# Kernel optimization log

Hardware: AMD Instinct MI355X
Metric: run time of the kernel (lower is better)

The kernel has to match this reference:

```python
import jax, jax.numpy as jnp
import numpy as np
import math

B, S, D, H, DFF = 2, 2048, 1024, 16, 4096
DK = D // H
EPS = 1e-5

def layer_norm(x, g, b):
    mu = jnp.mean(x, axis=-1, keepdims=True)
    var = jnp.mean(jnp.square(x - mu), axis=-1, keepdims=True)
    return (x - mu) * jax.lax.rsqrt(var + EPS) * g + b

def setup_inputs() -> dict:
    key = jax.random.key(0)
    ks = jax.random.split(key, 12)
    p = lambda k, shape: (jax.random.normal(k, shape, jnp.float32) * 0.02)
    return {
        "x": jax.random.normal(ks[0], (B, S, D), jnp.float32),
        "mask": jax.random.randint(ks[1], (B, S, S), 0, 2).astype(bool),
        "Wq": p(ks[2], (D, D)), "bq": jnp.zeros((D,), jnp.float32),
        "Wk": p(ks[3], (D, D)), "bk": jnp.zeros((D,), jnp.float32),
        "Wv": p(ks[4], (D, D)), "bv": jnp.zeros((D,), jnp.float32),
        "Wo": p(ks[5], (D, D)), "bo": jnp.zeros((D,), jnp.float32),
        "W1": p(ks[6], (DFF, D)), "b1": jnp.zeros((DFF,), jnp.float32),
        "W2": p(ks[7], (D, DFF)), "b2": jnp.zeros((D,), jnp.float32),
        "g_attn": jnp.ones((D,), jnp.float32), "b_attn": jnp.zeros((D,), jnp.float32),
        "g_ffn": jnp.ones((D,), jnp.float32), "b_ffn": jnp.zeros((D,), jnp.float32),
    }

def reference(x, mask, Wq, bq, Wk, bk, Wv, bv, Wo, bo, W1, b1, W2, b2, g_attn, b_attn, g_ffn, b_ffn):
    orig_dtype = x.dtype
    nx = layer_norm(x, g_attn, b_attn)
    # project and split heads: [B,S,D] -> [B,H,S,DK]
    split = lambda t: t.reshape(B, S, H, DK).transpose(0, 2, 1, 3)
    q = split(nx @ Wq.T + bq)
    k = split(nx @ Wk.T + bk)
    v = split(nx @ Wv.T + bv)
    # explicit fp32 upcast as in the original
    scores = jnp.einsum('bhqd,bhkd->bhqk', q.astype(jnp.float32), k.astype(jnp.float32)) / math.sqrt(DK)
    scores = jnp.where(mask[:, None, :, :], jnp.float32(-10000.0), scores)
    attn = jax.nn.softmax(scores, axis=-1)
    context = jnp.einsum('bhqk,bhkd->bhqd', attn, v.astype(jnp.float32)).astype(orig_dtype)
    context = context.transpose(0, 2, 1, 3).reshape(B, S, D)
    x = x + (context @ Wo.T + bo)
    nx = layer_norm(x, g_ffn, b_ffn)
    h = jax.nn.gelu(nx @ W1.T + b1, approximate=False)  # torch F.gelu default is exact erf
    x = x + (h @ W2.T + b2)
    return x
```

## Files before the change

### kernel.cpp

```cpp
#include <hip/hip_runtime.h>
#include <stdint.h>

#define B_ 2
#define S_ 2048
#define D_ 1024
#define H_ 16
#define DK_ 64
#define DFF_ 4096
#define M_ (B_*S_)

typedef __bf16 bf16x8 __attribute__((ext_vector_type(8)));
typedef float  f32x4  __attribute__((ext_vector_type(4)));

__device__ __forceinline__ unsigned short f2bf(float f) {
    union { float f; unsigned int u; } x; x.f = f;
    unsigned int r = x.u + 0x7FFFu + ((x.u >> 16) & 1u);
    return (unsigned short)(r >> 16);
}
__device__ __forceinline__ float bf2f(unsigned short h) {
    union { unsigned int u; float f; } x; x.u = ((unsigned int)h) << 16;
    return x.f;
}

__device__ __forceinline__ void gl16(const void* g, void* l) {
    __builtin_amdgcn_global_load_lds((const __attribute__((address_space(1))) unsigned int*)g,
                                     (__attribute__((address_space(3))) unsigned int*)l, 16, 0, 0);
}

static constexpr size_t OFS_XC   = 256;
static constexpr size_t OFS_MASK = OFS_XC   + 8388608;
static constexpr size_t OFS_WQKV = OFS_MASK + 8388608;
static constexpr size_t OFS_WO   = OFS_WQKV + 6291456;
static constexpr size_t OFS_W1   = OFS_WO   + 2097152;
static constexpr size_t OFS_W2   = OFS_W1   + 8388608;
static constexpr size_t OFS_BIAS = OFS_W2   + 8388608;
static constexpr size_t OFS_S0   = OFS_BIAS + 53248;
static constexpr size_t OFS_S1   = OFS_S0   + 8388608;
static constexpr size_t OFS_S2   = OFS_S1   + 8388608;
static constexpr size_t OFS_S3   = OFS_S2   + 8388608;
static constexpr size_t OFS_H    = OFS_S3   + 8388608;

#define BOF_QKV 0
#define BOF_O   3072
#define BOF_2   4096
#define BOF_GA  5120
#define BOF_BA  6144
#define BOF_GF  7168
#define BOF_BF  8192
#define BOF_1   9216

struct Parts { float* p[4]; };

__global__ void detect_kernel(const unsigned int* __restrict__ g_attn,
                              const unsigned int* __restrict__ mask,
                              int* __restrict__ flags) {
    const int u = threadIdx.x;
    unsigned int w0 = mask[u], w1 = mask[64 + u];
    bool a32  = (w0 <= 1u) && (w1 <= 1u);
    bool af32 = ((w0 == 0u) || (w0 == 0x3F800000u)) && ((w1 == 0u) || (w1 == 0x3F800000u));
    bool a8 = true;
    #pragma unroll
    for (int j = 0; j < 4; j++)
        a8 = a8 && (((w0 >> (8*j)) & 0xFFu) <= 1u) && (((w1 >> (8*j)) & 0xFFu) <= 1u);
    int all32 = __all(a32), all8 = __all(a8), allf32 = __all(af32);
    if (u == 0) {
        unsigned int g0 = g_attn[0];
        int fm = (g0 == 0x3F800000u) ? 0 : ((g0 == 0x3C003C00u) ? 2 : 1);
        int mm = all32 ? 0 : (all8 ? 1 : (allf32 ? 2 : 3));
        flags[0] = fm; flags[1] = mm;
    }
}

struct BigSrc { const void* s[7]; };

__device__ __forceinline__ void conv4(const void* src, size_t si,
                                      unsigned short* dst, size_t di, int fm) {
    ushort4 ov;
    if (fm == 1) {
        ov = *(const ushort4*)((const unsigned short*)src + si);
    } else if (fm == 0) {
        const float* fp = (const float*)src + si;
        float4 f = *(const float4*)fp;
        ov.x = f2bf(f.x); ov.y = f2bf(f.y); ov.z = f2bf(f.z); ov.w = f2bf(f.w);
    } else {
        const _Float16* hp = (const _Float16*)src + si;
        ov.x = f2bf((float)hp[0]); ov.y = f2bf((float)hp[1]);
        ov.z = f2bf((float)hp[2]); ov.w = f2bf((float)hp[3]);
    }
    *(ushort4*)(dst + di) = ov;
}

__global__ __launch_bounds__(256) void convert_big_kernel(BigSrc srcs, char* ws) {
    const int fm = ((const int*)ws)[0];
    size_t i = ((size_t)blockIdx.x * 256 + threadIdx.x) * 4;
    if (i >= 16777216) return;
    if (i < 4194304) {
        conv4(srcs.s[0], i, (unsigned short*)(ws + OFS_XC), i, fm);
    } else if (i < 7340032) {
        size_t off = i - 4194304;
        int sub = (int)(off >> 20);
        size_t loc = off & 1048575;
        conv4(srcs.s[1 + sub], loc, (unsigned short*)(ws + OFS_WQKV), off, fm);
    } else if (i < 8388608) {
        size_t off = i - 7340032;
        conv4(srcs.s[4], off, (unsigned short*)(ws + OFS_WO), off, fm);
    } else if (i < 12582912) {
        size_t off = i - 8388608;
        conv4(srcs.s[5], off, (unsigned short*)(ws + OFS_W1), off, fm);
    } else {
        size_t off = i - 12582912;
        conv4(srcs.s[6], off, (unsigned short*)(ws + OFS_W2), off, fm);
    }
}

struct SmallSrc { const void* s[10]; };

__global__ __launch_bounds__(256) void convert_small_kernel(SmallSrc srcs, char* ws) {
    int idx = blockIdx.x * 256 + threadIdx.x;
    if (idx >= 13312) return;
    const int fm = ((const int*)ws)[0];
    int seg = idx >> 10; if (seg > 9) seg = 9;
    int loc = idx - seg * 1024;
    const void* s = srcs.s[seg];
    float f;
    if (fm == 1)      f = bf2f(((const unsigned short*)s)[loc]);
    else if (fm == 0) f = ((const float*)s)[loc];
    else              f = (float)((const _Float16*)s)[loc];
    ((float*)(ws + OFS_BIAS))[idx] = f;
}

__global__ __launch_bounds__(256) void mask_bits_kernel(const void* msrc, char* ws) {
    const int mm = ((const int*)ws)[1];
    size_t e = (size_t)blockIdx.x * 256 + threadIdx.x;
    bool p;
    if (mm == 0)      p = ((const int*)msrc)[e] != 0;
    else if (mm == 1) p = ((const unsigned char*)msrc)[e] != 0;
    else if (mm == 2) p = ((const unsigned int*)msrc)[e] != 0;
    else              p = ((const unsigned short*)msrc)[e] != 0;
    unsigned long long bal = __ballot(p);
    if ((threadIdx.x & 63) == 0)
        ((unsigned long long*)(ws + OFS_MASK))[e >> 6] = bal;
}

template<int IN32>
__global__ __launch_bounds__(256) void ln_kernel(const void* __restrict__ xin,
                                                 const float* __restrict__ g,
                                                 const float* __restrict__ b,
                                                 unsigned short* __restrict__ out) {
    const int row = blockIdx.x;
    const int t = threadIdx.x;
    float f0, f1, f2, f3;
    if (IN32) {
        const float* xr = (const float*)xin + (size_t)row * D_;
        float4 xv = *(const float4*)(xr + t * 4);
        f0 = xv.x; f1 = xv.y; f2 = xv.z; f3 = xv.w;
    } else {
        const unsigned short* xr = (const unsigned short*)xin + (size_t)row * D_;
        ushort4 xv = *(const ushort4*)(xr + t * 4);
        f0 = bf2f(xv.x); f1 = bf2f(xv.y); f2 = bf2f(xv.z); f3 = bf2f(xv.w);
    }
    float s = f0 + f1 + f2 + f3;
    float q = f0*f0 + f1*f1 + f2*f2 + f3*f3;
    for (int m = 1; m < 64; m <<= 1) { s += __shfl_xor(s, m); q += __shfl_xor(q, m); }
    __shared__ float red[8];
    __shared__ float mv[2];
    int w = t >> 6, u = t & 63;
    if (u == 0) { red[w*2] = s; red[w*2+1] = q; }
    __syncthreads();
    if (t == 0) {
        float S = red[0] + red[2] + red[4] + red[6];
        float Q = red[1] + red[3] + red[5] + red[7];
        float mu = S * (1.0f / D_);
        float var = Q * (1.0f / D_) - mu * mu;
        mv[0] = mu; mv[1] = rsqrtf(var + 1e-5f);
    }
    __syncthreads();
    float mu = mv[0], r = mv[1];
    int i = t * 4;
    ushort4 ov;
    ov.x = f2bf((f0 - mu) * r * g[i]   + b[i]);
    ov.y = f2bf((f1 - mu) * r * g[i+1] + b[i+1]);
    ov.z = f2bf((f2 - mu) * r * g[i+2] + b[i+2]);
    ov.w = f2bf((f3 - mu) * r * g[i+3] + b[i+3]);
    *(ushort4*)(out + (size_t)row * D_ + i) = ov;
}

template<int EPI>
__global__ __launch_bounds__(256) void gemm_bt_kernel(
    const unsigned short* __restrict__ A,
    const unsigned short* __restrict__ Bm,
    const float* __restrict__ bias,
    void* __restrict__ out,
    float* __restrict__ p1,
    unsigned short* __restrict__ q_out,
    unsigned short* __restrict__ k_out,
    unsigned short* __restrict__ vT_out,
    int M, int N, int K, int Kstride)
{
    __shared__ __attribute__((aligned(16))) unsigned short ldsA[2][4096];
    __shared__ __attribute__((aligned(16))) unsigned short ldsB[2][4096];
    const int t = threadIdx.x;
    const int w = t >> 6, u = t & 63, quad = u >> 4, l15 = u & 15;
    const int bx = blockIdx.x, by = blockIdx.y;
    const int z = (EPI == 5) ? blockIdx.z : 0;

    const int c0 = t, c1 = t + 256;
    const int ar0 = by*128 + ((c0 >> 6) << 4) + (c0 & 15), ak0 = ((c0 >> 4) & 3) * 8;
    const int ar1 = by*128 + ((c1 >> 6) << 4) + (c1 & 15), ak1 = ((c1 >> 4) & 3) * 8;
    const int br0 = bx*128 + ((c0 >> 6) << 4) + (c0 & 15);
    const int br1 = bx*128 + ((c1 >> 6) << 4) + (c1 & 15);
    const size_t kofs = (size_t)z * K;
    const unsigned short* pa0 = A  + (size_t)ar0 * Kstride + kofs + ak0;
    const unsigned short* pa1 = A  + (size_t)ar1 * Kstride + kofs + ak1;
    const unsigned short* pb0 = Bm + (size_t)br0 * Kstride + kofs + ak0;
    const unsigned short* pb1 = Bm + (size_t)br1 * Kstride + kofs + ak1;

    const int cbase0 = (w * 64) * 8;
    const int cbase1 = (256 + w * 64) * 8;

    f32x4 acc[4][4];
    #pragma unroll
    for (int i = 0; i < 4; i++)
        #pragma unroll
        for (int j = 0; j < 4; j++) acc[i][j] = (f32x4){0.f, 0.f, 0.f, 0.f};

    const int mbase = (w >> 1) * 4;
    const int nbase = (w & 1) * 4;

    for (int k0 = 0; k0 < K; k0 += 64) {
        __syncthreads();
        gl16(pa0,      &ldsA[0][cbase0]);
        gl16(pa1,      &ldsA[0][cbase1]);
        gl16(pb0,      &ldsB[0][cbase0]);
        gl16(pb1,      &ldsB[0][cbase1]);
        gl16(pa0 + 32, &ldsA[1][cbase0]);
        gl16(pa1 + 32, &ldsA[1][cbase1]);
        gl16(pb0 + 32, &ldsB[1][cbase0]);
        gl16(pb1 + 32, &ldsB[1][cbase1]);
        pa0 += 64; pa1 += 64; pb0 += 64; pb1 += 64;
        __syncthreads();
        #pragma unroll
        for (int sub = 0; sub < 2; sub++) {
            bf16x8 af[4], bfr[4];
            #pragma unroll
            for (int mt = 0; mt < 4; mt++) af[mt]  = *(const bf16x8*)&ldsA[sub][((mbase+mt)*64 + u) * 8];
            #pragma unroll
            for (int nt = 0; nt < 4; nt++) bfr[nt] = *(const bf16x8*)&ldsB[sub][((nbase+nt)*64 + u) * 8];
            #pragma unroll
            for (int mt = 0; mt < 4; mt++)
                #pragma unroll
                for (int nt = 0; nt < 4; nt++)
                    acc[mt][nt] = __builtin_amdgcn_mfma_f32_16x16x32_bf16(af[mt], bfr[nt], acc[mt][nt], 0, 0, 0);
        }
    }

    #pragma unroll
    for (int mt = 0; mt < 4; mt++) {
        #pragma unroll
        for (int nt = 0; nt < 4; nt++) {
            const int m0 = by*128 + (w >> 1)*64 + mt*16 + quad*4;
            const int n  = bx*128 + (w & 1)*64 + nt*16 + l15;
            float bn = 0.f;
            if constexpr (EPI != 5) bn = bias[n];
            float val[4];
            #pragma unroll
            for (int r = 0; r < 4; r++) val[r] = acc[mt][nt][r] + bn;
            if constexpr (EPI == 1) {
                #pragma unroll
                for (int r = 0; r < 4; r++) {
                    float v = val[r];
                    float ge = 0.5f * v * (1.0f + erff(v * 0.70710678118654752f));
                    ((unsigned short*)out)[(size_t)(m0 + r) * N + n] = f2bf(ge);
                }
            } else if constexpr (EPI == 2) {
                int sel = n >> 10, nn = n & 1023;
                int hh = nn >> 6, dk = nn & 63;
                int bb = m0 >> 11, ss = m0 & 2047;
                if (sel < 2) {
                    unsigned short* dst = sel == 0 ? q_out : k_out;
                    #pragma unroll
                    for (int r = 0; r < 4; r++)
                        dst[(((size_t)bb * H_ + hh) * S_ + ss + r) * DK_ + dk] = f2bf(val[r]);
                } else {
                    ushort4 pk;
                    pk.x = f2bf(val[0]); pk.y = f2bf(val[1]);
                    pk.z = f2bf(val[2]); pk.w = f2bf(val[3]);
                    *(ushort4*)&vT_out[(((size_t)bb * H_ + hh) * DK_ + dk) * S_ + ss] = pk;
                }
            } else {
                float* dst = z ? p1 : (float*)out;
                #pragma unroll
                for (int r = 0; r < 4; r++)
                    dst[(size_t)(m0 + r) * N + n] = val[r];
            }
        }
    }
}

template<int EPI>
__global__ __launch_bounds__(512, 2) void gemm256_kernel(
    const unsigned short* __restrict__ A,
    const unsigned short* __restrict__ Bm,
    const float* __restrict__ bias,
    void* __restrict__ out,
    unsigned short* __restrict__ q_out,
    unsigned short* __restrict__ k_out,
    unsigned short* __restrict__ vT_out,
    Parts parts,
    int N, int K, int Kstride)
{
    __shared__ __attribute__((aligned(16))) unsigned short sh[2][2][16384];
    const int t = threadIdx.x, w = t >> 6, u = t & 63, quad = u >> 4, l15 = u & 15;
    const int wm = w >> 2, wn = w & 3;
    const int bx = blockIdx.x, by = blockIdx.y;
    const int z = (EPI == 5) ? blockIdx.z : 0;
    const size_t kofs = (size_t)z * K;

    const int r1 = t >> 3, cc1 = t & 7, cs1 = cc1 ^ (r1 & 7);
    const unsigned short* srcA = A  + ((size_t)by * 256 + r1) * Kstride + kofs + cs1 * 8;
    const unsigned short* srcB = Bm + ((size_t)bx * 256 + r1) * Kstride + kofs + cs1 * 8;
    const size_t halfstep = 128 * (size_t)Kstride;
    const size_t rowstep64 = 64 * (size_t)Kstride;

    const int rowA = wm * 16 + l15;
    const int rowB = wn * 16 + l15;
    const int cx0 = ((quad    ) ^ (l15 & 7)) * 8;
    const int cx1 = ((quad + 4) ^ (l15 & 7)) * 8;

    f32x4 acc[8][4];
    #pragma unroll
    for (int i = 0; i < 8; i++)
        #pragma unroll
        for (int j = 0; j < 4; j++) acc[i][j] = (f32x4){0.f, 0.f, 0.f, 0.f};

#define STAGE(bufi, mat, half, tile) { \
    const unsigned short* _s = ((mat) ? srcB : srcA) + (size_t)(half) * halfstep + (size_t)(tile) * 64; \
    unsigned short* _d = &sh[bufi][mat][(half) * 8192 + w * 512]; \
    gl16(_s, _d); gl16(_s + rowstep64, _d + 4096); }

#define LOAD_A(bufi, mh) { \
    const unsigned short* _p = &sh[bufi][0][0]; \
    _Pragma("unroll") \
    for (int f = 0; f < 4; f++) { \
        aF[f][0] = *(const bf16x8*)&_p[((mh) * 128 + f * 32 + rowA) * 64 + cx0]; \
        aF[f][1] = *(const bf16x8*)&_p[((mh) * 128 + f * 32 + rowA) * 64 + cx1]; \
    } }

#define LOAD_B(bufi, nh) { \
    const unsigned short* _p = &sh[bufi][1][0]; \
    _Pragma("unroll") \
    for (int g = 0; g < 2; g++) { \
        bF[nh][g][0] = *(const bf16x8*)&_p[((nh) * 128 + g * 64 + rowB) * 64 + cx0]; \
        bF[nh][g][1] = *(const bf16x8*)&_p[((nh) * 128 + g * 64 + rowB) * 64 + cx1]; \
    } }

#define QUADC(mh, nh) \
    __builtin_amdgcn_s_setprio(1); \
    _Pragma("unroll") \
    for (int ks = 0; ks < 2; ks++) \
        _Pragma("unroll") \
        for (int f = 0; f < 4; f++) \
            _Pragma("unroll") \
            for (int g = 0; g < 2; g++) \
                acc[(mh)*4 + f][(nh)*2 + g] = __builtin_amdgcn_mfma_f32_16x16x32_bf16( \
                    aF[f][ks], bF[nh][g][ks], acc[(mh)*4 + f][(nh)*2 + g], 0, 0, 0); \
    __builtin_amdgcn_s_setprio(0);

#define BARR __builtin_amdgcn_s_barrier()
#define VM6  asm volatile("s_waitcnt vmcnt(6)" ::: "memory")

    STAGE(0, 0, 0, 0);
    STAGE(0, 1, 0, 0);
    STAGE(0, 0, 1, 0);
    STAGE(0, 1, 1, 0);
    STAGE(1, 0, 0, 1);
    STAGE(1, 1, 0, 1);
    STAGE(1, 0, 1, 1);
    VM6;
    BARR;

    bf16x8 aF[4][2];
    bf16x8 bF[2][2][2];

    const int nIt = K >> 7;
    const int lastT = (K >> 6) - 1;

    #pragma unroll 1
    for (int it = 0; it < nIt; ++it) {
        const int t1 = 2 * it + 1;
        const int t2 = (it < nIt - 1) ? 2 * it + 2 : lastT;
        const int t3 = (it < nIt - 1) ? 2 * it + 3 : lastT;

        LOAD_A(0, 0); LOAD_B(0, 0);
        STAGE(1, 1, 1, t1);
        BARR; QUADC(0, 0); BARR;
        LOAD_B(0, 1);
        STAGE(0, 0, 0, t2);
        BARR; QUADC(0, 1); BARR;
        LOAD_A(0, 1);
        STAGE(0, 1, 0, t2);
        BARR; QUADC(1, 0); BARR;
        STAGE(0, 0, 1, t2);
        VM6;
        BARR; QUADC(1, 1); BARR;
        LOAD_A(1, 0); LOAD_B(1, 0);
        STAGE(0, 1, 1, t2);
        BARR; QUADC(0, 0); BARR;
        LOAD_B(1, 1);
        STAGE(1, 0, 0, t3);
        BARR; QUADC(0, 1); BARR;
        LOAD_A(1, 1);
        STAGE(1, 1, 0, t3);
        BARR; QUADC(1, 0); BARR;
        STAGE(1, 0, 1, t3);
        VM6;
        BARR; QUADC(1, 1); BARR;
    }
    asm volatile("s_waitcnt vmcnt(0)" ::: "memory");

#undef STAGE
#undef LOAD_A
#undef LOAD_B
#undef QUADC
#undef BARR
#undef VM6

    if constexpr (EPI == 1) {
        #pragma unroll
        for (int f = 0; f < 8; f++) {
            #pragma unroll
            for (int g = 0; g < 4; g++) {
                const int m0 = by * 256 + f * 32 + wm * 16 + quad * 4;
                const int n  = bx * 256 + g * 64 + wn * 16 + l15;
                const float bn = bias[n];
                #pragma unroll
                for (int r = 0; r < 4; r++) {
                    float v = acc[f][g][r] + bn;
                    float ge = 0.5f * v * (1.0f + erff(v * 0.70710678118654752f));
                    ((unsigned short*)out)[(size_t)(m0 + r) * N + n] = f2bf(ge);
                }
            }
        }
    } else if constexpr (EPI == 2) {
        const int sel = bx >> 2;
        #pragma unroll
        for (int f = 0; f < 8; f++) {
            #pragma unroll
            for (int g = 0; g < 4; g++) {
                const int m0 = by * 256 + f * 32 + wm * 16 + quad * 4;
                const int n  = bx * 256 + g * 64 + wn * 16 + l15;
                const float bn = bias[n];
                const int nn = n & 1023, hh = nn >> 6, dk = nn & 63;
                const int bb = m0 >> 11, ss = m0 & 2047;
                if (sel < 2) {
                    unsigned short* dst = sel == 0 ? q_out : k_out;
                    #pragma unroll
                    for (int r = 0; r < 4; r++)
                        dst[(((size_t)bb * H_ + hh) * S_ + ss + r) * DK_ + dk] = f2bf(acc[f][g][r] + bn);
                } else {
                    ushort4 pk;
                    pk.x = f2bf(acc[f][g][0] + bn); pk.y = f2bf(acc[f][g][1] + bn);
                    pk.z = f2bf(acc[f][g][2] + bn); pk.w = f2bf(acc[f][g][3] + bn);
                    *(ushort4*)&vT_out[(((size_t)bb * H_ + hh) * DK_ + dk) * S_ + ss] = pk;
                }
            }
        }
    } else {
        float* dst = parts.p[z];
        #pragma unroll
        for (int f = 0; f < 8; f++) {
            #pragma unroll
            for (int g = 0; g < 4; g++) {
                const int m0 = by * 256 + f * 32 + wm * 16 + quad * 4;
                const int n  = bx * 256 + g * 64 + wn * 16 + l15;
                #pragma unroll
                for (int r = 0; r < 4; r++)
                    dst[(size_t)(m0 + r) * N + n] = acc[f][g][r];
            }
        }
    }
}

template<int FINAL>
__global__ __launch_bounds__(256) void reduce_kernel(
    const float* __restrict__ p0, const float* __restrict__ p1,
    const float* __restrict__ bias, const void* __restrict__ res,
    void* __restrict__ out, const int* __restrict__ flags)
{
    size_t i = ((size_t)blockIdx.x * 256 + threadIdx.x) * 4;
    int n = (int)(i & 1023);
    float4 a = *(const float4*)(p0 + i);
    float4 b = *(const float4*)(p1 + i);
    const float4 bi = *(const float4*)(bias + n);
    float v0 = a.x + b.x + bi.x, v1 = a.y + b.y + bi.y;
    float v2 = a.z + b.z + bi.z, v3 = a.w + b.w + bi.w;
    if constexpr (FINAL == 0) {
        ushort4 rr = *(const ushort4*)((const unsigned short*)res + i);
        v0 += bf2f(rr.x); v1 += bf2f(rr.y); v2 += bf2f(rr.z); v3 += bf2f(rr.w);
        float4 ov = {v0, v1, v2, v3};
        *(float4*)((float*)out + i) = ov;
    } else {
        float4 rr = *(const float4*)((const float*)res + i);
        v0 += rr.x; v1 += rr.y; v2 += rr.z; v3 += rr.w;
        const int fm = flags[0];
        if (fm == 0) {
            float4 ov = {v0, v1, v2, v3};
            *(float4*)((float*)out + i) = ov;
        } else if (fm == 2) {
            _Float16* op = (_Float16*)out + i;
            op[0] = (_Float16)v0; op[1] = (_Float16)v1;
            op[2] = (_Float16)v2; op[3] = (_Float16)v3;
        } else {
            ushort4 ov;
            ov.x = f2bf(v0); ov.y = f2bf(v1); ov.z = f2bf(v2); ov.w = f2bf(v3);
            *(ushort4*)((unsigned short*)out + i) = ov;
        }
    }
}

__global__ __launch_bounds__(256) void reduce4_kernel(
    Parts parts, const float* __restrict__ bias, const float* __restrict__ res,
    void* __restrict__ out, const int* __restrict__ flags)
{
    size_t i = ((size_t)blockIdx.x * 256 + threadIdx.x) * 4;
    int n = (int)(i & 1023);
    float4 a = *(const float4*)(parts.p[0] + i);
    float4 b = *(const float4*)(parts.p[1] + i);
    float4 c = *(const float4*)(parts.p[2] + i);
    float4 d = *(const float4*)(parts.p[3] + i);
    const float4 bi = *(const float4*)(bias + n);
    float4 rr = *(const float4*)(res + i);
    float v0 = (a.x + b.x) + (c.x + d.x) + bi.x + rr.x;
    float v1 = (a.y + b.y) + (c.y + d.y) + bi.y + rr.y;
    float v2 = (a.z + b.z) + (c.z + d.z) + bi.z + rr.z;
    float v3 = (a.w + b.w) + (c.w + d.w) + bi.w + rr.w;
    const int fm = flags[0];
    if (fm == 0) {
        float4 ov = {v0, v1, v2, v3};
        *(float4*)((float*)out + i) = ov;
    } else if (fm == 2) {
        _Float16* op = (_Float16*)out + i;
        op[0] = (_Float16)v0; op[1] = (_Float16)v1;
        op[2] = (_Float16)v2; op[3] = (_Float16)v3;
    } else {
        ushort4 ov;
        ov.x = f2bf(v0); ov.y = f2bf(v1); ov.z = f2bf(v2); ov.w = f2bf(v3);
        *(ushort4*)((unsigned short*)out + i) = ov;
    }
}

__global__ __launch_bounds__(512) void attn_kernel(
    const unsigned short* __restrict__ q,
    const unsigned short* __restrict__ k,
    const unsigned short* __restrict__ vT,
    const unsigned long long* __restrict__ mb,
    unsigned short* __restrict__ ctx)
{
    const int blk = blockIdx.x;
    const int xcd = blk & 7;
    const int slot = blk >> 3;
    const int qt = slot & 15;
    const int pg = slot >> 4;
    const int p  = xcd + 8 * pg;
    const int h = p & 15, b = p >> 4;
    const int bh = b * H_ + h;

    const int t = threadIdx.x, w = t >> 6, u = t & 63, quad = u >> 4, l15 = u & 15;

    __shared__ __attribute__((aligned(16))) unsigned short Kt[512 * 8];
    __shared__ __attribute__((aligned(16))) unsigned short Vt[512 * 8];
    __shared__ __attribute__((aligned(16))) unsigned short Pw[8][16 * 72];

    const size_t base = (size_t)bh * S_ * DK_;
    const int qr0 = qt * 128 + w * 16;

    bf16x8 aq[2];
    #pragma unroll
    for (int hf = 0; hf < 2; hf++)
        aq[hf] = *(const bf16x8*)(q + base + (size_t)(qr0 + l15) * DK_ + hf*32 + quad*8);

    const int sr = t >> 3, sc = (t & 7) ^ (sr & 7);
    const unsigned short* kp = k  + base + (size_t)sr * DK_ + sc * 8;
    const unsigned short* vp = vT + base + (size_t)sr * S_  + sc * 8;
    unsigned short* lk = &Kt[(w * 64) * 8];
    unsigned short* lv = &Vt[(w * 64) * 8];

    f32x4 o[4];
    #pragma unroll
    for (int nt = 0; nt < 4; nt++) o[nt] = (f32x4){0.f, 0.f, 0.f, 0.f};
    float ls[4] = {0.f, 0.f, 0.f, 0.f};
    const float C = 0.125f * 1.4426950408889634f;

    for (int kt = 0; kt < S_ / 64; kt++) {
        unsigned long long m64[4];
        #pragma unroll
        for (int r = 0; r < 4; r++)
            m64[r] = mb[((size_t)b * S_ + qr0 + quad*4 + r) * 32 + kt];

        __syncthreads();
        gl16(kp, lk);
        gl16(vp, lv);
        kp += 64 * DK_;
        vp += 64;
        __syncthreads();

        f32x4 s4[4];
        #pragma unroll
        for (int nt = 0; nt < 4; nt++) s4[nt] = (f32x4){0.f, 0.f, 0.f, 0.f};
        #pragma unroll
        for (int nt = 0; nt < 4; nt++) {
            int rr = nt * 16 + l15;
            #pragma unroll
            for (int hf = 0; hf < 2; hf++) {
                int cc = (hf * 4 + quad) ^ (rr & 7);
                bf16x8 bk = *(const bf16x8*)&Kt[(rr * 8 + cc) * 8];
                s4[nt] = __builtin_amdgcn_mfma_f32_16x16x32_bf16(aq[hf], bk, s4[nt], 0, 0, 0);
            }
        }

        #pragma unroll
        for (int r = 0; r < 4; r++) {
            unsigned int lo = (unsigned int)m64[r], hi = (unsigned int)(m64[r] >> 32);
            #pragma unroll
            for (int nt = 0; nt < 4; nt++) {
                unsigned int word = (nt & 2) ? hi : lo;
                unsigned int bit = (word >> ((nt & 1) * 16 + l15)) & 1u;
                float arg = bit ? -20000.0f : s4[nt][r] * C;
                float e = exp2f(arg);
                ls[r] += e;
                Pw[w][(quad * 4 + r) * 72 + nt * 16 + l15] = f2bf(e);
            }
        }

        #pragma unroll
        for (int ks = 0; ks < 2; ks++) {
            bf16x8 ap = *(const bf16x8*)&Pw[w][l15 * 72 + ks * 32 + quad * 8];
            #pragma unroll
            for (int nt = 0; nt < 4; nt++) {
                int rr = nt * 16 + l15;
                int cc = (ks * 4 + quad) ^ (rr & 7);
                bf16x8 bv = *(const bf16x8*)&Vt[(rr * 8 + cc) * 8];
                o[nt] = __builtin_amdgcn_mfma_f32_16x16x32_bf16(ap, bv, o[nt], 0, 0, 0);
            }
        }
    }

    #pragma unroll
    for (int r = 0; r < 4; r++) {
        float l = ls[r];
        l += __shfl_xor(l, 1); l += __shfl_xor(l, 2);
        l += __shfl_xor(l, 4); l += __shfl_xor(l, 8);
        float inv = 1.0f / l;
        int qg = qr0 + quad * 4 + r;
        #pragma unroll
        for (int nt = 0; nt < 4; nt++)
            ctx[((size_t)b * S_ + qg) * D_ + h * DK_ + nt * 16 + l15] = f2bf(o[nt][r] * inv);
    }
}

extern "C" void kernel_launch(void* const* d_in, const int* in_sizes, int n_in,
                              void* d_out, int out_size, void* d_ws, size_t ws_size,
                              hipStream_t stream) {
    char* ws = (char*)d_ws;

    detect_kernel<<<1, 64, 0, stream>>>((const unsigned int*)d_in[14],
                                        (const unsigned int*)d_in[1], (int*)ws);

    BigSrc bs; bs.s[0] = d_in[0]; bs.s[1] = d_in[2]; bs.s[2] = d_in[4];
    bs.s[3] = d_in[6]; bs.s[4] = d_in[8]; bs.s[5] = d_in[10]; bs.s[6] = d_in[12];
    convert_big_kernel<<<16384, 256, 0, stream>>>(bs, ws);

    SmallSrc ss;
    ss.s[0] = d_in[3];  ss.s[1] = d_in[5];  ss.s[2] = d_in[7];  ss.s[3] = d_in[9];
    ss.s[4] = d_in[13]; ss.s[5] = d_in[14]; ss.s[6] = d_in[15]; ss.s[7] = d_in[16];
    ss.s[8] = d_in[17]; ss.s[9] = d_in[11];
    convert_small_kernel<<<52, 256, 0, stream>>>(ss, ws);

    mask_bits_kernel<<<32768, 256, 0, stream>>>(d_in[1], ws);

    const unsigned short* xc  = (const unsigned short*)(ws + OFS_XC);
    const unsigned short* wqk = (const unsigned short*)(ws + OFS_WQKV);
    const unsigned short* wo  = (const unsigned short*)(ws + OFS_WO);
    const unsigned short* w1  = (const unsigned short*)(ws + OFS_W1);
    const unsigned short* w2  = (const unsigned short*)(ws + OFS_W2);
    float* biasf = (float*)(ws + OFS_BIAS);
    unsigned short* nx1 = (unsigned short*)(ws + OFS_S0);
    unsigned short* ctx = (unsigned short*)(ws + OFS_S0);
    unsigned short* nx2 = (unsigned short*)(ws + OFS_S0);
    unsigned short* qb  = (unsigned short*)(ws + OFS_S1);
    unsigned short* kb  = (unsigned short*)(ws + OFS_S2);
    unsigned short* vTb = (unsigned short*)(ws + OFS_S3);
    float*          x2f = (float*)(ws + OFS_S2);
    unsigned short* hb  = (unsigned short*)(ws + OFS_H);
    float* opart0 = (float*)(ws + OFS_H);
    float* opart1 = (float*)(ws + OFS_H + 16777216);
    const unsigned long long* mbits = (const unsigned long long*)(ws + OFS_MASK);
    const int* flags = (const int*)ws;

    Parts noparts = {};

    ln_kernel<0><<<4096, 256, 0, stream>>>(xc, biasf + BOF_GA, biasf + BOF_BA, nx1);

    gemm256_kernel<2><<<dim3(12, 16), 512, 0, stream>>>(
        nx1, wqk, biasf + BOF_QKV, nullptr, qb, kb, vTb, noparts, 3072, 1024, 1024);

    attn_kernel<<<512, 512, 0, stream>>>(qb, kb, vTb, mbits, ctx);

    gemm_bt_kernel<5><<<dim3(8, 32, 2), 256, 0, stream>>>(
        ctx, wo, nullptr, opart0, opart1, nullptr, nullptr, nullptr, M_, 1024, 512, 1024);
    reduce_kernel<0><<<4096, 256, 0, stream>>>(
        opart0, opart1, biasf + BOF_O, xc, x2f, flags);

    ln_kernel<1><<<4096, 256, 0, stream>>>(x2f, biasf + BOF_GF, biasf + BOF_BF, nx2);

    gemm256_kernel<1><<<dim3(16, 16), 512, 0, stream>>>(
        nx2, w1, biasf + BOF_1, hb, nullptr, nullptr, nullptr, noparts, 4096, 1024, 1024);

    float* fp3 = nullptr;
    if (ws_size >= OFS_H + 33554432 + 16777216)      fp3 = (float*)(ws + OFS_H + 33554432);
    else if ((size_t)out_size >= 16777216)           fp3 = (float*)d_out;

    if (fp3) {
        Parts pp;
        pp.p[0] = (float*)(ws + OFS_XC);
        pp.p[1] = (float*)(ws + OFS_S0);
        pp.p[2] = (float*)(ws + OFS_WQKV);
        pp.p[3] = fp3;
        gemm256_kernel<5><<<dim3(4, 16, 4), 512, 0, stream>>>(
            hb, w2, nullptr, nullptr, nullptr, nullptr, nullptr, pp, 1024, 1024, 4096);
        reduce4_kernel<<<4096, 256, 0, stream>>>(pp, biasf + BOF_2, x2f, d_out, flags);
    } else {
        float* fpart0 = (float*)(ws + OFS_XC);
        float* fpart1 = (float*)(ws + OFS_S0);
        gemm_bt_kernel<5><<<dim3(8, 32, 2), 256, 0, stream>>>(
            hb, w2, nullptr, fpart0, fpart1, nullptr, nullptr, nullptr, M_, 1024, 2048, 4096);
        reduce_kernel<1><<<4096, 256, 0, stream>>>(
            fpart0, fpart1, biasf + BOF_2, x2f, d_out, flags);
    }
}
```

Measured before the change: 431.9 us.

## Double-buffer K/V tiles in attention and pack bf16 conversion of probabilities

The attention kernel now keeps two LDS buffers for K and V and issues the global-to-LDS loads for the next tile before computing on the current one. Explicit vmcnt waits and raw barriers replace the two __syncthreads per iteration, so load latency can overlap the MFMA and exp work. The softmax step also converts probabilities with the packed v_cvt_pk_bf16_f32 instruction instead of software rounding. The cost is double the K/V shared memory, which may reduce occupancy, plus reliance on hand-tuned waitcnt counts, and the asm conversion may round differently from the old software path.

```diff
diff --git a/kernel.cpp b/kernel.cpp
--- a/kernel.cpp
+++ b/kernel.cpp
@@ -567,8 +567,8 @@
 
     const int t = threadIdx.x, w = t >> 6, u = t & 63, quad = u >> 4, l15 = u & 15;
 
-    __shared__ __attribute__((aligned(16))) unsigned short Kt[512 * 8];
-    __shared__ __attribute__((aligned(16))) unsigned short Vt[512 * 8];
+    __shared__ __attribute__((aligned(16))) unsigned short Kt[2][4096];
+    __shared__ __attribute__((aligned(16))) unsigned short Vt[2][4096];
     __shared__ __attribute__((aligned(16))) unsigned short Pw[8][16 * 72];
 
     const size_t base = (size_t)bh * S_ * DK_;
@@ -580,10 +580,8 @@
         aq[hf] = *(const bf16x8*)(q + base + (size_t)(qr0 + l15) * DK_ + hf*32 + quad*8);
 
     const int sr = t >> 3, sc = (t & 7) ^ (sr & 7);
-    const unsigned short* kp = k  + base + (size_t)sr * DK_ + sc * 8;
-    const unsigned short* vp = vT + base + (size_t)sr * S_  + sc * 8;
-    unsigned short* lk = &Kt[(w * 64) * 8];
-    unsigned short* lv = &Vt[(w * 64) * 8];
+    const unsigned short* kp0 = k  + base + (size_t)sr * DK_ + sc * 8;
+    const unsigned short* vp0 = vT + base + (size_t)sr * S_  + sc * 8;
 
     f32x4 o[4];
     #pragma unroll
@@ -591,18 +589,22 @@
     float ls[4] = {0.f, 0.f, 0.f, 0.f};
     const float C = 0.125f * 1.4426950408889634f;
 
+    gl16(kp0, &Kt[0][w * 512]);
+    gl16(vp0, &Vt[0][w * 512]);
+
+    #pragma unroll 1
     for (int kt = 0; kt < S_ / 64; kt++) {
+        const int buf = kt & 1;
         unsigned long long m64[4];
         #pragma unroll
         for (int r = 0; r < 4; r++)
             m64[r] = mb[((size_t)b * S_ + qr0 + quad*4 + r) * 32 + kt];
 
-        __syncthreads();
-        gl16(kp, lk);
-        gl16(vp, lv);
-        kp += 64 * DK_;
-        vp += 64;
-        __syncthreads();
+        const int nx = (kt < S_ / 64 - 1) ? kt + 1 : kt;
+        gl16(kp0 + (size_t)nx * (64 * DK_), &Kt[buf ^ 1][w * 512]);
+        gl16(vp0 + (size_t)nx * 64,         &Vt[buf ^ 1][w * 512]);
+        asm volatile("s_waitcnt vmcnt(6)" ::: "memory");
+        __builtin_amdgcn_s_barrier();
 
         f32x4 s4[4];
         #pragma unroll
@@ -613,7 +615,7 @@
             #pragma unroll
             for (int hf = 0; hf < 2; hf++) {
                 int cc = (hf * 4 + quad) ^ (rr & 7);
-                bf16x8 bk = *(const bf16x8*)&Kt[(rr * 8 + cc) * 8];
+                bf16x8 bk = *(const bf16x8*)&Kt[buf][(rr * 8 + cc) * 8];
                 s4[nt] = __builtin_amdgcn_mfma_f32_16x16x32_bf16(aq[hf], bk, s4[nt], 0, 0, 0);
             }
         }
@@ -621,15 +623,26 @@
         #pragma unroll
         for (int r = 0; r < 4; r++) {
             unsigned int lo = (unsigned int)m64[r], hi = (unsigned int)(m64[r] >> 32);
-            #pragma unroll
-            for (int nt = 0; nt < 4; nt++) {
-                unsigned int word = (nt & 2) ? hi : lo;
-                unsigned int bit = (word >> ((nt & 1) * 16 + l15)) & 1u;
-                float arg = bit ? -20000.0f : s4[nt][r] * C;
-                float e = exp2f(arg);
-                ls[r] += e;
-                Pw[w][(quad * 4 + r) * 72 + nt * 16 + l15] = f2bf(e);
+            float e0, e1, e2, e3;
+            {
+                unsigned int b0 = (lo >> l15) & 1u;
+                unsigned int b1 = (lo >> (16 + l15)) & 1u;
+                unsigned int b2 = (hi >> l15) & 1u;
+                unsigned int b3 = (hi >> (16 + l15)) & 1u;
+                e0 = exp2f(b0 ? -20000.0f : s4[0][r] * C);
+                e1 = exp2f(b1 ? -20000.0f : s4[1][r] * C);
+                e2 = exp2f(b2 ? -20000.0f : s4[2][r] * C);
+                e3 = exp2f(b3 ? -20000.0f : s4[3][r] * C);
             }
+            ls[r] += (e0 + e1) + (e2 + e3);
+            unsigned int pk01, pk23;
+            asm("v_cvt_pk_bf16_f32 %0, %1, %2" : "=v"(pk01) : "v"(e0), "v"(e1));
+            asm("v_cvt_pk_bf16_f32 %0, %1, %2" : "=v"(pk23) : "v"(e2), "v"(e3));
+            unsigned short* prow = &Pw[w][(quad * 4 + r) * 72 + l15];
+            prow[0]  = (unsigned short)pk01;
+            prow[16] = (unsigned short)(pk01 >> 16);
+            prow[32] = (unsigned short)pk23;
+            prow[48] = (unsigned short)(pk23 >> 16);
         }
 
         #pragma unroll
@@ -639,11 +652,14 @@
             for (int nt = 0; nt < 4; nt++) {
                 int rr = nt * 16 + l15;
                 int cc = (ks * 4 + quad) ^ (rr & 7);
-                bf16x8 bv = *(const bf16x8*)&Vt[(rr * 8 + cc) * 8];
+                bf16x8 bv = *(const bf16x8*)&Vt[buf][(rr * 8 + cc) * 8];
                 o[nt] = __builtin_amdgcn_mfma_f32_16x16x32_bf16(ap, bv, o[nt], 0, 0, 0);
             }
         }
-    }
+
+        __builtin_amdgcn_s_barrier();
+    }
+    asm volatile("s_waitcnt vmcnt(0)" ::: "memory");
 
     #pragma unroll
     for (int r = 0; r < 4; r++) {
```

After: 432.5 us. Within noise of the previous version (+0.1%).
